# Kernel optimization log

Measured on AMD Instinct MI355X. Metric: run time of the kernel, lower is better.

The kernel has to match this reference:

```python
import jax, jax.numpy as jnp
import numpy as np

H = 64
N_NODES = 12000
N_EDGES = 50000


def setup_inputs() -> dict:
    key = jax.random.key(0)
    ks = jax.random.split(key, 16)
    s = 1.0 / np.sqrt(H)
    inp = {
        "node": jax.random.normal(ks[0], (N_NODES, H), jnp.float32),
        "edge": jax.random.normal(ks[1], (N_EDGES, H), jnp.float32),
        "hidden_feats": jax.random.normal(ks[2], (N_NODES, H), jnp.float32),
        "src": jax.random.randint(ks[3], (N_EDGES,), 0, N_NODES, jnp.int32),
        "dst": jax.random.randint(ks[4], (N_EDGES,), 0, N_NODES, jnp.int32),
        # edge_network: Linear(H, 2H) -> ReLU -> Linear(2H, H*H)
        "W1": jax.random.uniform(ks[5], (2 * H, H), jnp.float32, -s, s),
        "b1": jax.random.uniform(ks[6], (2 * H,), jnp.float32, -s, s),
        "W2": jax.random.uniform(ks[7], (H * H, 2 * H), jnp.float32, -1 / np.sqrt(2 * H), 1 / np.sqrt(2 * H)),
        "b2": jax.random.uniform(ks[8], (H * H,), jnp.float32, -1 / np.sqrt(2 * H), 1 / np.sqrt(2 * H)),
        # GRUCell params (torch layout: [3H, H], gate order r,z,n)
        "W_ih": jax.random.uniform(ks[9], (3 * H, H), jnp.float32, -s, s),
        "W_hh": jax.random.uniform(ks[10], (3 * H, H), jnp.float32, -s, s),
        "b_ih": jax.random.uniform(ks[11], (3 * H,), jnp.float32, -s, s),
        "b_hh": jax.random.uniform(ks[12], (3 * H,), jnp.float32, -s, s),
        # LayerNorm params
        "gamma": jnp.ones((H,), jnp.float32),
        "beta": jnp.zeros((H,), jnp.float32),
    }
    return inp


def _gru_cell(x, h, W_ih, W_hh, b_ih, b_hh):
    gi = x @ W_ih.T + b_ih  # [N, 3H]
    gh = h @ W_hh.T + b_hh  # [N, 3H]
    r = jax.nn.sigmoid(gi[:, :H] + gh[:, :H])
    z = jax.nn.sigmoid(gi[:, H:2 * H] + gh[:, H:2 * H])
    n = jnp.tanh(gi[:, 2 * H:] + r * gh[:, 2 * H:])
    return (1.0 - z) * n + z * h


def reference(node, edge, hidden_feats, src, dst, W1, b1, W2, b2,
              W_ih, W_hh, b_ih, b_hh, gamma, beta):
    n_nodes = node.shape[0]
    # edge network -> per-edge [H,H] weight matrices
    eh = jax.nn.relu(edge @ W1.T + b1)                      # [E, 2H]
    Wedge = (eh @ W2.T + b2).reshape(-1, H, H)              # [E, H, H]
    # gather src feats, per-edge matmul (row-vector @ matrix), scatter-sum to dst
    msg = jnp.einsum('eh,ehk->ek', node[src], Wedge)        # [E, H]
    agg = jax.ops.segment_sum(msg, dst, num_segments=n_nodes)  # [N, H]
    new_node_feats = jax.nn.relu(agg)
    out = _gru_cell(new_node_feats, hidden_feats, W_ih, W_hh, b_ih, b_hh)
    # LayerNorm (eps=1e-5)
    mu = jnp.mean(out, axis=-1, keepdims=True)
    var = jnp.var(out, axis=-1, keepdims=True)
    out = (out - mu) * jax.lax.rsqrt(var + 1e-5) * gamma + beta
    return out
```

## Files before the change

kernel.cpp:

```cpp
#include <hip/hip_runtime.h>

#define H 64
#define NEDGE 50000
#define NNODE 12000
#define EPAD 50176

typedef _Float16 f16;
typedef _Float16 h8 __attribute__((ext_vector_type(8)));
typedef float f4 __attribute__((ext_vector_type(4)));
typedef float fv16 __attribute__((ext_vector_type(16)));

#define O_EDGEH 0ull
#define O_W2G   6422528ull
#define O_B2G   7471104ull
#define O_W1G   7479296ull
#define O_WG    7495680ull
#define O_AGG   7561216ull

__device__ __forceinline__ void async16(const void* g, void* l) {
  __builtin_amdgcn_global_load_lds((const __attribute__((address_space(1))) void*)g,
                                   (__attribute__((address_space(3))) void*)l, 16, 0, 0);
}

__device__ __forceinline__ fv16 zero16() {
  fv16 z;
#pragma unroll
  for (int i = 0; i < 16; ++i) z[i] = 0.f;
  return z;
}

__global__ __launch_bounds__(256) void k_prep(const float* __restrict__ edge, const float* __restrict__ W1,
                                              const float* __restrict__ W2, const float* __restrict__ b2,
                                              const float* __restrict__ Wih, const float* __restrict__ Whh,
                                              f16* __restrict__ edgeh, f16* __restrict__ w1g, f16* __restrict__ w2g,
                                              f16* __restrict__ b2g, f16* __restrict__ wg, float* __restrict__ agg) {
  int bid = blockIdx.x;
  int t = threadIdx.x;
  if (bid < 750) {
    int id = bid * 256 + t;
    *(f4*)(agg + (long)id * 4) = (f4){0.f, 0.f, 0.f, 0.f};
    return;
  }
  if (bid < 2318) {
    long id8 = (long)(bid - 750) * 256 + t;
    long e = id8 >> 3;
    int c = (int)(id8 & 7) * 8;
    h8 o = {};
    if (e < NEDGE) {
      const float* p = edge + e * 64 + c;
      f4 v0 = *(const f4*)p, v1 = *(const f4*)(p + 4);
#pragma unroll
      for (int j = 0; j < 4; ++j) { o[j] = (f16)v0[j]; o[4 + j] = (f16)v1[j]; }
    }
    *(h8*)(edgeh + e * 64 + c) = o;
    return;
  }
  if (bid < 4366) {
    int id = (bid - 2318) * 256 + t;
    int i = id & 7, l = (id >> 3) & 63, nh = (id >> 9) & 1, s = (id >> 10) & 7, h = id >> 13;
    int n = nh * 32 + (l & 31), j = s * 16 + ((l >> 5) << 3) + i;
    w2g[id] = (f16)W2[(h * 64 + n) * 128 + j];
    return;
  }
  if (bid < 4382) {
    int id = (bid - 4366) * 256 + t;
    int i = id & 7, l = (id >> 3) & 63, nh = (id >> 9) & 1, s = id >> 10;
    int n = nh * 32 + (l & 31), k = s * 16 + ((l >> 5) << 3) + i;
    b2g[id] = (f16)b2[k * 64 + n];
    return;
  }
  if (bid < 4414) {
    int id = (bid - 4382) * 256 + t;
    int i = id & 7, l = (id >> 3) & 63, nt = (id >> 9) & 3, s = id >> 11;
    int n = nt * 32 + (l & 31), k = s * 16 + ((l >> 5) << 3) + i;
    w1g[id] = (f16)W1[n * 64 + k];
    return;
  }
  {
    int id = (bid - 4414) * 256 + t;
    int ii = id & 7, l = (id >> 3) & 63, tt = (id >> 9) & 15, s = id >> 13;
    int k = s * 32 + ((l >> 4) << 3) + ii, n = tt * 16 + (l & 15);
    float v;
    if (n < 128) v = (k < 64) ? Wih[n * 64 + k] : Whh[n * 64 + (k - 64)];
    else if (n < 192) v = (k < 64) ? Wih[n * 64 + k] : 0.f;
    else v = (k < 64) ? 0.f : Whh[(n - 64) * 64 + (k - 64)];
    wg[id] = (f16)v;
  }
}

__global__ __launch_bounds__(256, 3) void k_msg(const float* __restrict__ node,
                                                const int* __restrict__ src, const int* __restrict__ dst,
                                                const f16* __restrict__ edgeh, const f16* __restrict__ w1g,
                                                const f16* __restrict__ w2g, const float* __restrict__ b1,
                                                float* __restrict__ agg) {
  __shared__ __align__(16) char lds[52736];
  f16* eh_s = (f16*)lds;
  char* bbuf = lds;
  f16* vT = (f16*)(lds + 32768);
  int* ssrc = (int*)(lds + 51200);
  int* sdst = (int*)(lds + 51712);
  float* b1s = (float*)(lds + 52224);

  int t = threadIdx.x;
  int bid = blockIdx.x;
  int e_base = (bid >> 1) * 128;
  int hs = bid & 1;

  if (t < 128) {
    int eg = e_base + t;
    bool valid = eg < NEDGE;
    ssrc[t] = valid ? src[eg] : 0;
    sdst[t] = valid ? dst[eg] : 0;
  } else {
    b1s[t - 128] = b1[t - 128];
  }
  {
    int e = t >> 1, half = t & 1;
    int eg = e_base + e;
    int si = (eg < NEDGE) ? src[eg] : 0;
    const f4* nr = (const f4*)(node + (long)si * 64 + half * 32);
#pragma unroll
    for (int b = 0; b < 4; ++b) {
      f4 v0 = nr[b * 2], v1 = nr[b * 2 + 1];
      h8 pk;
#pragma unroll
      for (int m = 0; m < 4; ++m) { pk[m] = (f16)v0[m]; pk[4 + m] = (f16)v1[m]; }
      *(h8*)(vT + e * 72 + (half * 4 + b) * 8) = pk;
    }
  }
  __syncthreads();

  int wave = t >> 6, lane = t & 63;
  int wm = wave & 1, wn = wave >> 1;
  int l31 = lane & 31, lh = lane >> 5;

  {
    h8 afr[2][4];
#pragma unroll
    for (int mt = 0; mt < 2; ++mt)
#pragma unroll
      for (int s = 0; s < 4; ++s)
        afr[mt][s] = *(const h8*)(edgeh + (long)(e_base + wm * 64 + mt * 32 + l31) * 64 + s * 16 + lh * 8);
    h8 bfr[2][4];
#pragma unroll
    for (int nt = 0; nt < 2; ++nt)
#pragma unroll
      for (int s = 0; s < 4; ++s)
        bfr[nt][s] = *(const h8*)(w1g + ((s * 4 + wn * 2 + nt) * 64 + lane) * 8);
    fv16 acc_eh[2][2];
#pragma unroll
    for (int mt = 0; mt < 2; ++mt)
#pragma unroll
      for (int nt = 0; nt < 2; ++nt) acc_eh[mt][nt] = zero16();
#pragma unroll
    for (int s = 0; s < 4; ++s)
#pragma unroll
      for (int mt = 0; mt < 2; ++mt)
#pragma unroll
        for (int nt = 0; nt < 2; ++nt)
          acc_eh[mt][nt] = __builtin_amdgcn_mfma_f32_32x32x16_f16(afr[mt][s], bfr[nt][s], acc_eh[mt][nt], 0, 0, 0);
#pragma unroll
    for (int mt = 0; mt < 2; ++mt)
#pragma unroll
      for (int nt = 0; nt < 2; ++nt)
#pragma unroll
        for (int r = 0; r < 16; ++r) {
          int row = (r & 3) + 8 * (r >> 2) + 4 * lh;
          int e = wm * 64 + mt * 32 + row;
          int n = wn * 64 + nt * 32 + l31;
          float val = fmaxf(acc_eh[mt][nt][r] + b1s[n], 0.f);
          int o = n >> 3;
          eh_s[e * 128 + ((o ^ (e & 15)) << 3) + (n & 7)] = (f16)val;
        }
  }
  __syncthreads();

  h8 ehreg[2][8];
#pragma unroll
  for (int mt = 0; mt < 2; ++mt) {
    int e = wm * 64 + mt * 32 + l31;
#pragma unroll
    for (int s = 0; s < 8; ++s) {
      int o = (s * 2 + lh) ^ (e & 15);
      ehreg[mt][s] = *(const h8*)(eh_s + e * 128 + o * 8);
    }
  }
  __syncthreads();

  const char* w2b = (const char*)w2g;
  int h0 = hs << 5;
#pragma unroll
  for (int r = 0; r < 4; ++r) async16(w2b + (long)h0 * 16384 + r * 4096 + t * 16, bbuf + r * 4096 + t * 16);

  fv16 acc[2];
  acc[0] = zero16(); acc[1] = zero16();
  const f16* vrow0 = vT + (wm * 64 + l31) * 72;
  const f16* vrow1 = vT + (wm * 64 + 32 + l31) * 72;

#pragma unroll 1
  for (int hb = hs * 4; hb < hs * 4 + 4; ++hb) {
    h8 vh0 = *(const h8*)(vrow0 + hb * 8);
    h8 vh1 = *(const h8*)(vrow1 + hb * 8);
#pragma unroll
    for (int hh = 0; hh < 8; ++hh) {
      int h = hb * 8 + hh;
      __syncthreads();
      if (h != 31 || hs) {
        const char* gsrc = w2b + (long)(h + 1) * 16384;
        char* ldst = bbuf + ((h + 1) & 1) * 16384;
#pragma unroll
        for (int r = 0; r < 4; ++r) async16(gsrc + r * 4096 + t * 16, ldst + r * 4096 + t * 16);
      }
      const f16* bp = (const f16*)(bbuf + (h & 1) * 16384) + (wn * 64 + lane) * 8;
      f16 v0 = vh0[hh], v1 = vh1[hh];
#pragma unroll
      for (int s = 0; s < 8; ++s) {
        h8 bf = *(const h8*)(bp + s * 1024);
        h8 a0 = ehreg[0][s] * v0;
        acc[0] = __builtin_amdgcn_mfma_f32_32x32x16_f16(a0, bf, acc[0], 0, 0, 0);
        h8 a1 = ehreg[1][s] * v1;
        acc[1] = __builtin_amdgcn_mfma_f32_32x32x16_f16(a1, bf, acc[1], 0, 0, 0);
      }
    }
  }
  if (hs) {
    __syncthreads();
    const f16* bp = (const f16*)bbuf + (wn * 64 + lane) * 8;
#pragma unroll
    for (int s = 0; s < 4; ++s) {
      h8 bf = *(const h8*)(bp + s * 1024);
      h8 a0 = *(const h8*)(vrow0 + (s * 2 + lh) * 8);
      h8 a1 = *(const h8*)(vrow1 + (s * 2 + lh) * 8);
      acc[0] = __builtin_amdgcn_mfma_f32_32x32x16_f16(a0, bf, acc[0], 0, 0, 0);
      acc[1] = __builtin_amdgcn_mfma_f32_32x32x16_f16(a1, bf, acc[1], 0, 0, 0);
    }
  }

  int n = wn * 32 + l31;
#pragma unroll
  for (int mt = 0; mt < 2; ++mt)
#pragma unroll
    for (int r = 0; r < 16; ++r) {
      int el = wm * 64 + mt * 32 + (r & 3) + 8 * (r >> 2) + 4 * lh;
      if (e_base + el < NEDGE)
        atomicAdd(&agg[(long)sdst[el] * 64 + n], acc[mt][r]);
    }
}

__global__ __launch_bounds__(256) void k_node(const float* __restrict__ agg, const float* __restrict__ hid,
                                              const f16* __restrict__ wg,
                                              const float* __restrict__ bih, const float* __restrict__ bhh,
                                              const float* __restrict__ gamma, const float* __restrict__ beta,
                                              float* __restrict__ out) {
  __shared__ __align__(16) f16 xh_s[128 * 136];
  __shared__ float bsum[128], bin_s[64], bhn_s[64], gam_s[64], bet_s[64];
  int t = threadIdx.x;
  int n0 = blockIdx.x * 128;

  if (t < 128) bsum[t] = bih[t] + bhh[t];
  else if (t < 192) bin_s[t - 128] = bih[t];
  else bhn_s[t - 192] = bhh[t - 64];
  if (t < 64) gam_s[t] = gamma[t];
  else if (t < 128) bet_s[t - 64] = beta[t - 64];

  {
    int m = t >> 1, half = t & 1;
    int mg = n0 + m;
    bool vld = mg < NNODE;
    const float* sp = half ? (hid + (long)mg * 64) : (agg + (long)mg * 64);
#pragma unroll
    for (int jj = 0; jj < 8; ++jj) {
      f4 v0 = {0, 0, 0, 0}, v1 = {0, 0, 0, 0};
      if (vld) { v0 = *(const f4*)(sp + jj * 8); v1 = *(const f4*)(sp + jj * 8 + 4); }
      h8 pk;
#pragma unroll
      for (int m2 = 0; m2 < 4; ++m2) {
        pk[m2] = (f16)(half ? v0[m2] : fmaxf(v0[m2], 0.f));
        pk[4 + m2] = (f16)(half ? v1[m2] : fmaxf(v1[m2], 0.f));
      }
      *(h8*)(xh_s + m * 136 + half * 64 + jj * 8) = pk;
    }
  }
  __syncthreads();

  int wave = t >> 6, lane = t & 63;
  int l15 = lane & 15, lq = lane >> 4;

  f4 acc[2][16];
#pragma unroll
  for (int g = 0; g < 2; ++g)
#pragma unroll
    for (int tt = 0; tt < 16; ++tt) acc[g][tt] = (f4){0.f, 0.f, 0.f, 0.f};

#pragma unroll
  for (int s = 0; s < 4; ++s) {
    h8 a0 = *(const h8*)(xh_s + (wave * 32 + l15) * 136 + s * 32 + lq * 8);
    h8 a1 = *(const h8*)(xh_s + (wave * 32 + 16 + l15) * 136 + s * 32 + lq * 8);
#pragma unroll
    for (int tt = 0; tt < 16; ++tt) {
      h8 b = *(const h8*)(wg + ((s * 16 + tt) * 64 + lane) * 8);
      acc[0][tt] = __builtin_amdgcn_mfma_f32_16x16x32_f16(a0, b, acc[0][tt], 0, 0, 0);
      acc[1][tt] = __builtin_amdgcn_mfma_f32_16x16x32_f16(a1, b, acc[1][tt], 0, 0, 0);
    }
  }

#pragma unroll
  for (int g = 0; g < 2; ++g)
#pragma unroll
    for (int r = 0; r < 4; ++r) {
      int mg = n0 + wave * 32 + g * 16 + lq * 4 + r;
      bool vld = mg < NNODE;
      float o[4], ssum = 0.f, s2 = 0.f;
#pragma unroll
      for (int t0 = 0; t0 < 4; ++t0) {
        int f = t0 * 16 + l15;
        float rpre = acc[g][t0][r] + bsum[f];
        float zpre = acc[g][4 + t0][r] + bsum[64 + f];
        float ginv = acc[g][8 + t0][r] + bin_s[f];
        float ghnv = acc[g][12 + t0][r] + bhn_s[f];
        float rr = 1.f / (1.f + __expf(-rpre));
        float zz = 1.f / (1.f + __expf(-zpre));
        float hv = vld ? hid[(long)mg * 64 + f] : 0.f;
        float nn = tanhf(ginv + rr * ghnv);
        float oo = (1.f - zz) * nn + zz * hv;
        o[t0] = oo; ssum += oo; s2 += oo * oo;
      }
#pragma unroll
      for (int d = 1; d < 16; d <<= 1) {
        ssum += __shfl_xor(ssum, d);
        s2 += __shfl_xor(s2, d);
      }
      float mu = ssum * (1.f / 64.f);
      float var = s2 * (1.f / 64.f) - mu * mu;
      float rstd = rsqrtf(var + 1e-5f);
      if (vld)
#pragma unroll
        for (int t0 = 0; t0 < 4; ++t0) {
          int f = t0 * 16 + l15;
          out[(long)mg * 64 + f] = (o[t0] - mu) * rstd * gam_s[f] + bet_s[f];
        }
    }
}

extern "C" void kernel_launch(void* const* d_in, const int* in_sizes, int n_in,
                              void* d_out, int out_size, void* d_ws, size_t ws_size,
                              hipStream_t stream) {
  const float* node = (const float*)d_in[0];
  const float* edge = (const float*)d_in[1];
  const float* hid = (const float*)d_in[2];
  const int* src = (const int*)d_in[3];
  const int* dst = (const int*)d_in[4];
  const float* W1 = (const float*)d_in[5];
  const float* b1 = (const float*)d_in[6];
  const float* W2 = (const float*)d_in[7];
  const float* b2 = (const float*)d_in[8];
  const float* Wih = (const float*)d_in[9];
  const float* Whh = (const float*)d_in[10];
  const float* bih = (const float*)d_in[11];
  const float* bhh = (const float*)d_in[12];
  const float* gamma = (const float*)d_in[13];
  const float* beta = (const float*)d_in[14];

  char* ws = (char*)d_ws;
  f16* edgeh = (f16*)(ws + O_EDGEH);
  f16* w2g = (f16*)(ws + O_W2G);
  f16* b2g = (f16*)(ws + O_B2G);
  f16* w1g = (f16*)(ws + O_W1G);
  f16* wg = (f16*)(ws + O_WG);
  float* agg = (float*)(ws + O_AGG);

  k_prep<<<4542, 256, 0, stream>>>(edge, W1, W2, b2, Wih, Whh, edgeh, w1g, w2g, b2g, wg, agg);
  k_msg<<<784, 256, 0, stream>>>(node, src, dst, edgeh, w1g, w2g, b1, agg);
  k_node<<<94, 256, 0, stream>>>(agg, hid, wg, bih, bhh, gamma, beta, (float*)d_out);
}
```

Measured before the change: 193.6 us.

## Split k across waves, stream W2 through registers, drop LDS double-buffer

The per-h W2 slice was staged into LDS with async copies and a block barrier every h step. Now each wave covers all 128 edges but only half of the k dimension, and prefetches its W2 fragments straight from global memory into registers, double-buffered across h. The barrier per h step goes away. In exchange, the two k-halves must be combined through an LDS reduction before the atomic scatter, and register use rises with four accumulators and eight B fragments, which may limit occupancy. Each wave also reads its B fragments directly from global or L2 memory instead of sharing one staged copy in LDS.

```diff
diff --git a/kernel.cpp b/kernel.cpp
--- a/kernel.cpp
+++ b/kernel.cpp
@@ -16,11 +16,6 @@
 #define O_W1G   7479296ull
 #define O_WG    7495680ull
 #define O_AGG   7561216ull
-
-__device__ __forceinline__ void async16(const void* g, void* l) {
-  __builtin_amdgcn_global_load_lds((const __attribute__((address_space(1))) void*)g,
-                                   (__attribute__((address_space(3))) void*)l, 16, 0, 0);
-}
 
 __device__ __forceinline__ fv16 zero16() {
   fv16 z;
@@ -93,13 +88,11 @@
                                                 const f16* __restrict__ edgeh, const f16* __restrict__ w1g,
                                                 const f16* __restrict__ w2g, const float* __restrict__ b1,
                                                 float* __restrict__ agg) {
-  __shared__ __align__(16) char lds[52736];
+  __shared__ __align__(16) char lds[52224];
   f16* eh_s = (f16*)lds;
-  char* bbuf = lds;
   f16* vT = (f16*)(lds + 32768);
-  int* ssrc = (int*)(lds + 51200);
-  int* sdst = (int*)(lds + 51712);
-  float* b1s = (float*)(lds + 52224);
+  int* sdst = (int*)(lds + 51200);
+  float* b1s = (float*)(lds + 51712);
 
   int t = threadIdx.x;
   int bid = blockIdx.x;
@@ -108,9 +101,7 @@
 
   if (t < 128) {
     int eg = e_base + t;
-    bool valid = eg < NEDGE;
-    ssrc[t] = valid ? src[eg] : 0;
-    sdst[t] = valid ? dst[eg] : 0;
+    sdst[t] = (eg < NEDGE) ? dst[eg] : 0;
   } else {
     b1s[t - 128] = b1[t - 128];
   }
@@ -133,6 +124,7 @@
   int wave = t >> 6, lane = t & 63;
   int wm = wave & 1, wn = wave >> 1;
   int l31 = lane & 31, lh = lane >> 5;
+  int kh = wm;
 
   {
     h8 afr[2][4];
@@ -175,76 +167,116 @@
   }
   __syncthreads();
 
-  h8 ehreg[2][8];
-#pragma unroll
-  for (int mt = 0; mt < 2; ++mt) {
-    int e = wm * 64 + mt * 32 + l31;
-#pragma unroll
-    for (int s = 0; s < 8; ++s) {
-      int o = (s * 2 + lh) ^ (e & 15);
+  h8 ehreg[4][4];
+#pragma unroll
+  for (int mt = 0; mt < 4; ++mt) {
+    int e = mt * 32 + l31;
+#pragma unroll
+    for (int s = 0; s < 4; ++s) {
+      int o = ((kh * 4 + s) * 2 + lh) ^ (e & 15);
       ehreg[mt][s] = *(const h8*)(eh_s + e * 128 + o * 8);
     }
   }
   __syncthreads();
 
-  const char* w2b = (const char*)w2g;
-  int h0 = hs << 5;
-#pragma unroll
-  for (int r = 0; r < 4; ++r) async16(w2b + (long)h0 * 16384 + r * 4096 + t * 16, bbuf + r * 4096 + t * 16);
-
-  fv16 acc[2];
-  acc[0] = zero16(); acc[1] = zero16();
-  const f16* vrow0 = vT + (wm * 64 + l31) * 72;
-  const f16* vrow1 = vT + (wm * 64 + 32 + l31) * 72;
+  fv16 acc[4];
+#pragma unroll
+  for (int mt = 0; mt < 4; ++mt) acc[mt] = zero16();
+  const f16* vr[4];
+#pragma unroll
+  for (int mt = 0; mt < 4; ++mt) vr[mt] = vT + (mt * 32 + l31) * 72;
+
+  const f16* bb = w2g + kh * 4096 + wn * 512 + (long)lane * 8;
+  int hfirst = hs << 5;
+  int hlast = hfirst + 31;
+
+  h8 bA[4], bB[4];
+#pragma unroll
+  for (int s = 0; s < 4; ++s) bA[s] = *(const h8*)(bb + (long)hfirst * 8192 + s * 1024);
+
+  auto step = [&](h8 (&bc)[4], h8 (&bn)[4], int h, const f16 (&vcur)[4]) {
+    if (h < hlast) {
+      const f16* bp = bb + (long)(h + 1) * 8192;
+#pragma unroll
+      for (int s = 0; s < 4; ++s) bn[s] = *(const h8*)(bp + s * 1024);
+    }
+#pragma unroll
+    for (int s = 0; s < 4; ++s) {
+      h8 bf = bc[s];
+#pragma unroll
+      for (int mt = 0; mt < 4; ++mt) {
+        h8 a = ehreg[mt][s] * vcur[mt];
+        acc[mt] = __builtin_amdgcn_mfma_f32_32x32x16_f16(a, bf, acc[mt], 0, 0, 0);
+      }
+    }
+  };
 
 #pragma unroll 1
   for (int hb = hs * 4; hb < hs * 4 + 4; ++hb) {
-    h8 vh0 = *(const h8*)(vrow0 + hb * 8);
-    h8 vh1 = *(const h8*)(vrow1 + hb * 8);
+    h8 vh[4];
+#pragma unroll
+    for (int mt = 0; mt < 4; ++mt) vh[mt] = *(const h8*)(vr[mt] + hb * 8);
 #pragma unroll
     for (int hh = 0; hh < 8; ++hh) {
       int h = hb * 8 + hh;
-      __syncthreads();
-      if (h != 31 || hs) {
-        const char* gsrc = w2b + (long)(h + 1) * 16384;
-        char* ldst = bbuf + ((h + 1) & 1) * 16384;
-#pragma unroll
-        for (int r = 0; r < 4; ++r) async16(gsrc + r * 4096 + t * 16, ldst + r * 4096 + t * 16);
-      }
-      const f16* bp = (const f16*)(bbuf + (h & 1) * 16384) + (wn * 64 + lane) * 8;
-      f16 v0 = vh0[hh], v1 = vh1[hh];
-#pragma unroll
-      for (int s = 0; s < 8; ++s) {
-        h8 bf = *(const h8*)(bp + s * 1024);
-        h8 a0 = ehreg[0][s] * v0;
-        acc[0] = __builtin_amdgcn_mfma_f32_32x32x16_f16(a0, bf, acc[0], 0, 0, 0);
-        h8 a1 = ehreg[1][s] * v1;
-        acc[1] = __builtin_amdgcn_mfma_f32_32x32x16_f16(a1, bf, acc[1], 0, 0, 0);
-      }
-    }
-  }
+      f16 vcur[4];
+#pragma unroll
+      for (int mt = 0; mt < 4; ++mt) vcur[mt] = vh[mt][hh];
+      if (hh & 1) step(bB, bA, h, vcur);
+      else step(bA, bB, h, vcur);
+    }
+  }
+
   if (hs) {
+    const f16* bt = w2g + (long)64 * 8192 + kh * 2048 + wn * 512 + (long)lane * 8;
+#pragma unroll
+    for (int sw = 0; sw < 2; ++sw) {
+      h8 bf = *(const h8*)(bt + sw * 1024);
+#pragma unroll
+      for (int mt = 0; mt < 4; ++mt) {
+        h8 a = *(const h8*)(vr[mt] + ((kh * 2 + sw) * 2 + lh) * 8);
+        acc[mt] = __builtin_amdgcn_mfma_f32_32x32x16_f16(a, bf, acc[mt], 0, 0, 0);
+      }
+    }
+  }
+
+  {
+    float* red = (float*)lds;
+    float* mybase = red + (wn * 2 + kh) * 2048;
+    auto wr = [&](const fv16& a, int sl) {
+#pragma unroll
+      for (int r = 0; r < 4; ++r) {
+        f4 q = {a[4 * r], a[4 * r + 1], a[4 * r + 2], a[4 * r + 3]};
+        *(f4*)(mybase + sl * 1024 + r * 256 + lane * 4) = q;
+      }
+    };
+    if (!kh) { wr(acc[2], 0); wr(acc[3], 1); }
+    else { wr(acc[0], 0); wr(acc[1], 1); }
     __syncthreads();
-    const f16* bp = (const f16*)bbuf + (wn * 64 + lane) * 8;
-#pragma unroll
-    for (int s = 0; s < 4; ++s) {
-      h8 bf = *(const h8*)(bp + s * 1024);
-      h8 a0 = *(const h8*)(vrow0 + (s * 2 + lh) * 8);
-      h8 a1 = *(const h8*)(vrow1 + (s * 2 + lh) * 8);
-      acc[0] = __builtin_amdgcn_mfma_f32_32x32x16_f16(a0, bf, acc[0], 0, 0, 0);
-      acc[1] = __builtin_amdgcn_mfma_f32_32x32x16_f16(a1, bf, acc[1], 0, 0, 0);
-    }
-  }
-
-  int n = wn * 32 + l31;
-#pragma unroll
-  for (int mt = 0; mt < 2; ++mt)
-#pragma unroll
-    for (int r = 0; r < 16; ++r) {
-      int el = wm * 64 + mt * 32 + (r & 3) + 8 * (r >> 2) + 4 * lh;
-      if (e_base + el < NEDGE)
-        atomicAdd(&agg[(long)sdst[el] * 64 + n], acc[mt][r]);
-    }
+    const float* pb = red + (wn * 2 + (1 - kh)) * 2048;
+    auto rd = [&](fv16& a, int sl) {
+#pragma unroll
+      for (int r = 0; r < 4; ++r) {
+        f4 q = *(const f4*)(pb + sl * 1024 + r * 256 + lane * 4);
+        a[4 * r] += q[0]; a[4 * r + 1] += q[1]; a[4 * r + 2] += q[2]; a[4 * r + 3] += q[3];
+      }
+    };
+    if (!kh) { rd(acc[0], 0); rd(acc[1], 1); }
+    else { rd(acc[2], 0); rd(acc[3], 1); }
+  }
+
+  {
+    int n = wn * 32 + l31;
+    auto scat = [&](const fv16& a, int mt) {
+#pragma unroll
+      for (int r = 0; r < 16; ++r) {
+        int el = mt * 32 + (r & 3) + 8 * (r >> 2) + 4 * lh;
+        if (e_base + el < NEDGE) atomicAdd(&agg[(long)sdst[el] * 64 + n], a[r]);
+      }
+    };
+    if (!kh) { scat(acc[0], 0); scat(acc[1], 1); }
+    else { scat(acc[2], 2); scat(acc[3], 3); }
+  }
 }
 
 __global__ __launch_bounds__(256) void k_node(const float* __restrict__ agg, const float* __restrict__ hid,
```

After: 271.7 us. 1.4x slower.
